# Performance work log

Hardware: AMD Instinct MI355X
Metric: run time of the kernel (lower is better)

The kernel has to match this reference:

```python
import jax, jax.numpy as jnp
import numpy as np

B, S, D = 1, 2048, 2048
N_HEADS, N_KV_HEADS = 32, 8
HEAD_DIM = D // N_HEADS  # 64
N_REP = N_HEADS // N_KV_HEADS  # 4


def setup_inputs() -> dict:
    key = jax.random.key(0)
    ks = jax.random.split(key, 6)
    x = jax.random.normal(ks[0], (B, S, D), dtype=jnp.float32)
    # weights stored as [in, out] so projection is x @ W
    wq = jax.random.normal(ks[1], (D, N_HEADS * HEAD_DIM), dtype=jnp.float32) * 0.02
    wk = jax.random.normal(ks[2], (D, N_KV_HEADS * HEAD_DIM), dtype=jnp.float32) * 0.02
    wv = jax.random.normal(ks[3], (D, N_KV_HEADS * HEAD_DIM), dtype=jnp.float32) * 0.02
    wo = jax.random.normal(ks[4], (N_HEADS * HEAD_DIM, D), dtype=jnp.float32) * 0.02
    # RoPE tables: freqs_cis has shape (seqlen, head_dim//2)
    theta = 10000.0
    inv_freq = 1.0 / (theta ** (jnp.arange(0, HEAD_DIM, 2, dtype=jnp.float32) / HEAD_DIM))
    angles = jnp.arange(S, dtype=jnp.float32)[:, None] * inv_freq[None, :]  # [S, hd/2]
    freqs_cos = jnp.cos(angles)
    freqs_sin = jnp.sin(angles)
    # causal additive mask, broadcast to [b, h, q, k]
    mask = jnp.triu(jnp.full((S, S), -jnp.inf, dtype=jnp.float32), k=1)[None, None]
    return {"x": x, "wq": wq, "wk": wk, "wv": wv, "wo": wo,
            "freqs_cos": freqs_cos, "freqs_sin": freqs_sin, "mask": mask}


def _apply_rope(t, cos, sin):
    # t: [B, S, H, head_dim]; pairs (t[...,2i], t[...,2i+1]) form complex numbers
    tr = t[..., 0::2]
    ti = t[..., 1::2]
    c = cos[None, :, None, :]
    s = sin[None, :, None, :]
    out_r = tr * c - ti * s
    out_i = tr * s + ti * c
    return jnp.stack([out_r, out_i], axis=-1).reshape(t.shape)


def reference(x, wq, wk, wv, wo, freqs_cos, freqs_sin, mask):
    bsz, seqlen, _ = x.shape
    xq = (x @ wq).reshape(bsz, seqlen, N_HEADS, HEAD_DIM)
    xk = (x @ wk).reshape(bsz, seqlen, N_KV_HEADS, HEAD_DIM)
    xv = (x @ wv).reshape(bsz, seqlen, N_KV_HEADS, HEAD_DIM)
    xq = _apply_rope(xq, freqs_cos, freqs_sin)
    xk = _apply_rope(xk, freqs_cos, freqs_sin)
    # repeat_kv (GQA expansion): [b,s,kvh,d] -> [b,s,h,d]
    keys = jnp.repeat(xk, N_REP, axis=2)
    values = jnp.repeat(xv, N_REP, axis=2)
    scale = 1.0 / np.sqrt(HEAD_DIM)
    # scores: [b, h, q, k]
    scores = jnp.einsum('bqhd,bkhd->bhqk', xq, keys) * scale
    scores = scores + mask
    probs = jax.nn.softmax(scores.astype(jnp.float32), axis=-1).astype(x.dtype)
    out = jnp.einsum('bhqk,bkhd->bqhd', probs, values)
    out = out.reshape(bsz, seqlen, N_HEADS * HEAD_DIM)
    return out @ wo
```

## Files before the change

### kernel.cpp

```cpp
#include <hip/hip_runtime.h>
#include <hip/hip_bf16.h>

#define S_LEN 2048
#define D_MODEL 2048
#define N_HEADS 32
#define N_KV 8
#define HEAD_DIM 64
#define KV_DIM (N_KV * HEAD_DIM)
#define QKV_N (D_MODEL + 2 * KV_DIM)

typedef __bf16 bf16_t;
typedef __attribute__((ext_vector_type(8))) __bf16 bf16x8;
typedef __attribute__((ext_vector_type(4))) float f32x4;
typedef __attribute__((ext_vector_type(16))) float f32x16;
typedef __attribute__((ext_vector_type(4))) unsigned int uint4v;
typedef __attribute__((ext_vector_type(2))) unsigned int uint2v;

__device__ __forceinline__ void gload_lds16(const void* g, void* l) {
    __builtin_amdgcn_global_load_lds(
        (const __attribute__((address_space(1))) unsigned char*)g,
        (__attribute__((address_space(3))) unsigned char*)l,
        16, 0, 0);
}

__global__ __launch_bounds__(256) void transpose_convert(const float* __restrict__ src,
                                                         __hip_bfloat16* __restrict__ dst,
                                                         int R, int C) {
    __shared__ float tile[32][33];
    const int bx = blockIdx.x * 32;
    const int by = blockIdx.y * 32;
    const int tx = threadIdx.x;
    const int ty = threadIdx.y;
#pragma unroll
    for (int i = 0; i < 32; i += 8)
        tile[ty + i][tx] = src[(size_t)(by + ty + i) * C + bx + tx];
    __syncthreads();
#pragma unroll
    for (int i = 0; i < 32; i += 8)
        dst[(size_t)(bx + ty + i) * R + by + tx] = __float2bfloat16(tile[tx][ty + i]);
}

__global__ __launch_bounds__(256) void convert_bf16(const float* __restrict__ src,
                                                    __hip_bfloat16* __restrict__ dst) {
    const int i = (blockIdx.x * 256 + threadIdx.x) * 8;
    const float4 a = *reinterpret_cast<const float4*>(src + i);
    const float4 b = *reinterpret_cast<const float4*>(src + i + 4);
    bf16x8 r;
    r[0] = (__bf16)a.x; r[1] = (__bf16)a.y; r[2] = (__bf16)a.z; r[3] = (__bf16)a.w;
    r[4] = (__bf16)b.x; r[5] = (__bf16)b.y; r[6] = (__bf16)b.z; r[7] = (__bf16)b.w;
    *reinterpret_cast<bf16x8*>(dst + i) = r;
}

__global__ __launch_bounds__(256) void rope_qk(__hip_bfloat16* __restrict__ t,
                                               const float* __restrict__ cos_t,
                                               const float* __restrict__ sin_t) {
    const int idx = blockIdx.x * blockDim.x + threadIdx.x;
    const int i = idx & 31;
    const int hh = (idx >> 5) % (N_HEADS + N_KV);
    const int s = idx / (32 * (N_HEADS + N_KV));
    const float c = cos_t[s * 32 + i];
    const float sn = sin_t[s * 32 + i];
    int col; float scale;
    if (hh < N_HEADS) { col = hh * HEAD_DIM + 2 * i; scale = 0.125f * 1.44269504f; }
    else { col = D_MODEL + (hh - N_HEADS) * HEAD_DIM + 2 * i; scale = 1.0f; }
    __hip_bfloat16* p = &t[(size_t)s * QKV_N + col];
    const float re = __bfloat162float(p[0]);
    const float im = __bfloat162float(p[1]);
    p[0] = __float2bfloat16((re * c - im * sn) * scale);
    p[1] = __float2bfloat16((re * sn + im * c) * scale);
}

__global__ __launch_bounds__(256) void transpose_v(const __hip_bfloat16* __restrict__ QKV,
                                                   __hip_bfloat16* __restrict__ Vt) {
    __shared__ __align__(16) __bf16 tile[64][72];
    const int s0 = blockIdx.x * 64;
    const int hkv = blockIdx.y;
    const int tid = threadIdx.x;
    {
        const int r = tid >> 2;
        const int c0 = (tid & 3) * 16;
        const __hip_bfloat16* src = QKV + (size_t)(s0 + r) * QKV_N + D_MODEL + KV_DIM + hkv * HEAD_DIM + c0;
        *reinterpret_cast<bf16x8*>(&tile[r][c0]) = *reinterpret_cast<const bf16x8*>(src);
        *reinterpret_cast<bf16x8*>(&tile[r][c0 + 8]) = *reinterpret_cast<const bf16x8*>(src + 8);
    }
    __syncthreads();
    {
        const int d = tid >> 2;
        const int sc = (tid & 3) * 16;
        bf16x8 o0, o1;
#pragma unroll
        for (int j = 0; j < 8; ++j) { o0[j] = tile[sc + j][d]; o1[j] = tile[sc + 8 + j][d]; }
        __hip_bfloat16* dst = Vt + (size_t)(hkv * HEAD_DIM + d) * S_LEN + s0 + sc;
        *reinterpret_cast<bf16x8*>(dst) = o0;
        *reinterpret_cast<bf16x8*>(dst + 8) = o1;
    }
}

__device__ inline void storeC(__hip_bfloat16* p, float v) { *p = __float2bfloat16(v); }
__device__ inline void storeC(float* p, float v) { *p = v; }

template <typename OutT>
__global__ __launch_bounds__(256) void gemm_bt(const __hip_bfloat16* __restrict__ A,
                                               const __hip_bfloat16* __restrict__ Bt,
                                               OutT* __restrict__ C,
                                               int M, int N, int K) {
    __shared__ __align__(16) __bf16 As[2][128 * 64];
    __shared__ __align__(16) __bf16 Bs[2][128 * 64];
    const int tid = threadIdx.x;
    const int w = tid >> 6, l = tid & 63;
    const int wr = w >> 1, wc = w & 1;
    const int l4 = l >> 4, l15 = l & 15;
    const int bm = blockIdx.y * 128, bn = blockIdx.x * 128;

    f32x4 acc[4][4];
#pragma unroll
    for (int i = 0; i < 4; ++i)
#pragma unroll
        for (int j = 0; j < 4; ++j) acc[i][j] = (f32x4){0.f, 0.f, 0.f, 0.f};

    auto stage = [&](int buf, int k0) {
#pragma unroll
        for (int p = 0; p < 4; ++p) {
            const int chunk = p * 256 + tid;
            const int row = chunk >> 3;
            const int cs = (chunk & 7) ^ (row & 7);
            gload_lds16(&A[(size_t)(bm + row) * K + k0 + cs * 8], &As[buf][chunk * 8]);
            gload_lds16(&Bt[(size_t)(bn + row) * K + k0 + cs * 8], &Bs[buf][chunk * 8]);
        }
    };

    const int nk = K >> 6;
    stage(0, 0);
    asm volatile("s_waitcnt vmcnt(0)" ::: "memory");
    __builtin_amdgcn_s_barrier();

#pragma unroll 2
    for (int kt = 0; kt < nk; ++kt) {
        const int cur = kt & 1;
        if (kt + 1 < nk) stage(cur ^ 1, (kt + 1) * 64);
#pragma unroll
        for (int ks = 0; ks < 2; ++ks) {
            bf16x8 a[4], b[4];
#pragma unroll
            for (int mi = 0; mi < 4; ++mi) {
                const int rr = wr * 64 + mi * 16 + l15;
                a[mi] = *reinterpret_cast<const bf16x8*>(
                    &As[cur][rr * 64 + (((ks * 4 + l4) ^ (rr & 7))) * 8]);
            }
#pragma unroll
            for (int ni = 0; ni < 4; ++ni) {
                const int rr = wc * 64 + ni * 16 + l15;
                b[ni] = *reinterpret_cast<const bf16x8*>(
                    &Bs[cur][rr * 64 + (((ks * 4 + l4) ^ (rr & 7))) * 8]);
            }
#pragma unroll
            for (int mi = 0; mi < 4; ++mi)
#pragma unroll
                for (int ni = 0; ni < 4; ++ni)
                    acc[mi][ni] = __builtin_amdgcn_mfma_f32_16x16x32_bf16(a[mi], b[ni], acc[mi][ni], 0, 0, 0);
        }
        asm volatile("s_waitcnt vmcnt(0)" ::: "memory");
        __builtin_amdgcn_s_barrier();
    }
#pragma unroll
    for (int mi = 0; mi < 4; ++mi)
#pragma unroll
        for (int ni = 0; ni < 4; ++ni)
#pragma unroll
            for (int r = 0; r < 4; ++r) {
                const int row = bm + wr * 64 + mi * 16 + l4 * 4 + r;
                const int col = bn + wc * 64 + ni * 16 + l15;
                storeC(&C[(size_t)row * N + col], acc[mi][ni][r]);
            }
}

#if __has_builtin(__builtin_amdgcn_permlane32_swap)
__device__ __forceinline__ void plswap(unsigned& x, unsigned& y, int) {
    uint2v r = __builtin_amdgcn_permlane32_swap(x, y, false, false);
    x = r[0]; y = r[1];
}
#else
__device__ __forceinline__ void plswap(unsigned& x, unsigned& y, int hi) {
    const unsigned px = __shfl_xor(x, 32, 64);
    const unsigned py = __shfl_xor(y, 32, 64);
    const unsigned nx = hi ? py : x;
    const unsigned ny = hi ? y : px;
    x = nx; y = ny;
}
#endif

__device__ __forceinline__ unsigned cvtpk_bf16(float lo, float hi) {
    unsigned w;
    asm("v_cvt_pk_bf16_f32 %0, %1, %2" : "=v"(w) : "v"(lo), "v"(hi));
    return w;
}
__device__ __forceinline__ float swap_max(float v, int hi) {
    unsigned x = __builtin_bit_cast(unsigned, v), y = x;
    plswap(x, y, hi);
    return fmaxf(__builtin_bit_cast(float, x), __builtin_bit_cast(float, y));
}
__device__ __forceinline__ float swap_add(float v, int hi) {
    unsigned x = __builtin_bit_cast(unsigned, v), y = x;
    plswap(x, y, hi);
    return __builtin_bit_cast(float, x) + __builtin_bit_cast(float, y);
}
template <int R0>
__device__ __forceinline__ bf16x8 build_pfrag(const f32x16& s, int hi) {
    unsigned A0 = cvtpk_bf16(s[R0 + 0], s[R0 + 1]);
    unsigned A1 = cvtpk_bf16(s[R0 + 2], s[R0 + 3]);
    unsigned B0 = cvtpk_bf16(s[R0 + 4], s[R0 + 5]);
    unsigned B1 = cvtpk_bf16(s[R0 + 6], s[R0 + 7]);
    plswap(A0, B0, hi);
    plswap(A1, B1, hi);
    uint4v u; u[0] = A0; u[1] = A1; u[2] = B0; u[3] = B1;
    return __builtin_bit_cast(bf16x8, u);
}

__global__ __launch_bounds__(512) void attn_kernel(const __hip_bfloat16* __restrict__ QKV,
                                                   const __hip_bfloat16* __restrict__ Vt,
                                                   __hip_bfloat16* __restrict__ O,
                                                   __hip_bfloat16* __restrict__ Opart,
                                                   float* __restrict__ ms,
                                                   int split) {
    const int h = blockIdx.y;
    const int hkv = h >> 2;
    int qc = 0, sl = 0, gbase = 0, ns = 1;
    if (!split) {
        qc = 7 - (int)blockIdx.x;
    } else {
        const int x = (int)blockIdx.x;
        int cum = 0;
#pragma unroll
        for (int q = 0; q < 8; ++q) {
            const int n = q + 1;
            if (x >= cum && x < cum + n) { qc = q; sl = x - cum; gbase = cum; }
            cum += n;
        }
        ns = qc + 1;
    }
    const int ntf = 4 * (qc + 1);
    const int t0 = split ? sl * 4 : 0;
    const int t1 = split ? min(t0 + 4, ntf) : ntf;

    const int tid = threadIdx.x;
    const int w = tid >> 6, l = tid & 63;
    const int lq = l & 31, hi = l >> 5;
    const int q0w = qc * 256 + w * 32;
    const int qlane = q0w + lq;

    __shared__ __align__(16) __bf16 Ks[2][64 * 64];
    __shared__ __align__(16) __bf16 Vs[2][64 * 64];

    const __hip_bfloat16* Kg = QKV + D_MODEL + hkv * HEAD_DIM;
    const __hip_bfloat16* Vg = Vt + (size_t)hkv * HEAD_DIM * S_LEN;

    auto stage = [&](int buf, int kv0) {
        const int chunk = tid;
        const int r = chunk >> 3;
        const int cs = (chunk & 7) ^ (r & 7);
        gload_lds16(&Kg[(size_t)(kv0 + r) * QKV_N + cs * 8], &Ks[buf][chunk * 8]);
        gload_lds16(&Vg[(size_t)r * S_LEN + kv0 + cs * 8], &Vs[buf][chunk * 8]);
    };

    bf16x8 qf[4];
#pragma unroll
    for (int f = 0; f < 4; ++f)
        qf[f] = *reinterpret_cast<const bf16x8*>(
            &QKV[(size_t)qlane * QKV_N + h * HEAD_DIM + 16 * f + 8 * hi]);

    f32x16 o0, o1;
#pragma unroll
    for (int r = 0; r < 16; ++r) { o0[r] = 0.f; o1[r] = 0.f; }
    float m_run = -__builtin_inff(), s_run = 0.f;

    stage(0, t0 * 64);

#pragma unroll 1
    for (int t = t0; t < t1; ++t) {
        __syncthreads();
        if (t + 1 < t1) stage((t + 1 - t0) & 1, (t + 1) * 64);
        const int kv0 = t * 64;
        if (kv0 <= q0w + 31) {
            const __bf16* Kb = Ks[(t - t0) & 1];
            const __bf16* Vb = Vs[(t - t0) & 1];

            f32x16 s0, s1;
#pragma unroll
            for (int r = 0; r < 16; ++r) { s0[r] = 0.f; s1[r] = 0.f; }
            __builtin_amdgcn_s_setprio(1);
#pragma unroll
            for (int f = 0; f < 4; ++f) {
                const int rr0 = lq;
                const int rr1 = 32 + lq;
                const bf16x8 ka0 = *reinterpret_cast<const bf16x8*>(
                    &Kb[rr0 * 64 + (((2 * f + hi) ^ (rr0 & 7))) * 8]);
                const bf16x8 ka1 = *reinterpret_cast<const bf16x8*>(
                    &Kb[rr1 * 64 + (((2 * f + hi) ^ (rr1 & 7))) * 8]);
                s0 = __builtin_amdgcn_mfma_f32_32x32x16_bf16(ka0, qf[f], s0, 0, 0, 0);
                s1 = __builtin_amdgcn_mfma_f32_32x32x16_bf16(ka1, qf[f], s1, 0, 0, 0);
            }
            __builtin_amdgcn_s_setprio(0);
            if (kv0 + 63 > q0w) {
#pragma unroll
                for (int r = 0; r < 16; ++r) {
                    const int kvb = (r & 3) + 8 * (r >> 2) + 4 * hi;
                    if (kv0 + kvb > qlane) s0[r] = -__builtin_inff();
                    if (kv0 + 32 + kvb > qlane) s1[r] = -__builtin_inff();
                }
            }
            float ta = fmaxf(s0[0], s1[0]), tb = fmaxf(s0[1], s1[1]);
            float tc = fmaxf(s0[2], s1[2]), td = fmaxf(s0[3], s1[3]);
#pragma unroll
            for (int r = 4; r < 16; r += 4) {
                ta = fmaxf(ta, fmaxf(s0[r], s1[r]));
                tb = fmaxf(tb, fmaxf(s0[r + 1], s1[r + 1]));
                tc = fmaxf(tc, fmaxf(s0[r + 2], s1[r + 2]));
                td = fmaxf(td, fmaxf(s0[r + 3], s1[r + 3]));
            }
            const float m_row = swap_max(fmaxf(fmaxf(ta, tb), fmaxf(tc, td)), hi);

            if (!__all(m_row <= m_run + 8.0f)) {
                const float mnew = fmaxf(m_run, m_row);
                const float corr = exp2f(m_run - mnew);
                m_run = mnew;
                s_run *= corr;
#pragma unroll
                for (int r = 0; r < 16; ++r) { o0[r] *= corr; o1[r] *= corr; }
            }
#pragma unroll
            for (int r = 0; r < 16; ++r) {
                s0[r] = exp2f(s0[r] - m_run);
                s1[r] = exp2f(s1[r] - m_run);
            }
            float ua = s0[0] + s1[0], ub = s0[1] + s1[1];
            float uc = s0[2] + s1[2], ud = s0[3] + s1[3];
#pragma unroll
            for (int r = 4; r < 16; r += 4) {
                ua += s0[r] + s1[r];
                ub += s0[r + 1] + s1[r + 1];
                uc += s0[r + 2] + s1[r + 2];
                ud += s0[r + 3] + s1[r + 3];
            }
            s_run += swap_add((ua + ub) + (uc + ud), hi);

            bf16x8 pa[4];
            pa[0] = build_pfrag<0>(s0, hi);
            pa[1] = build_pfrag<8>(s0, hi);
            pa[2] = build_pfrag<0>(s1, hi);
            pa[3] = build_pfrag<8>(s1, hi);

            __builtin_amdgcn_s_setprio(1);
#pragma unroll
            for (int ks = 0; ks < 4; ++ks) {
                const int rv0 = lq;
                const int rv1 = 32 + lq;
                const bf16x8 va0 = *reinterpret_cast<const bf16x8*>(
                    &Vb[rv0 * 64 + (((2 * ks + hi) ^ (rv0 & 7))) * 8]);
                const bf16x8 va1 = *reinterpret_cast<const bf16x8*>(
                    &Vb[rv1 * 64 + (((2 * ks + hi) ^ (rv1 & 7))) * 8]);
                o0 = __builtin_amdgcn_mfma_f32_32x32x16_bf16(va0, pa[ks], o0, 0, 0, 0);
                o1 = __builtin_amdgcn_mfma_f32_32x32x16_bf16(va1, pa[ks], o1, 0, 0, 0);
            }
            __builtin_amdgcn_s_setprio(0);
        }
    }

    if (ns == 1) {
        const float inv = 1.0f / s_run;
        __hip_bfloat16* orow = O + (size_t)qlane * D_MODEL + h * HEAD_DIM;
#pragma unroll
        for (int rr = 0; rr < 4; ++rr) {
            {
                uint2v u;
                u[0] = cvtpk_bf16(o0[4 * rr] * inv, o0[4 * rr + 1] * inv);
                u[1] = cvtpk_bf16(o0[4 * rr + 2] * inv, o0[4 * rr + 3] * inv);
                *reinterpret_cast<uint2v*>(orow + 8 * rr + 4 * hi) = u;
            }
            {
                uint2v u;
                u[0] = cvtpk_bf16(o1[4 * rr] * inv, o1[4 * rr + 1] * inv);
                u[1] = cvtpk_bf16(o1[4 * rr + 2] * inv, o1[4 * rr + 3] * inv);
                *reinterpret_cast<uint2v*>(orow + 32 + 8 * rr + 4 * hi) = u;
            }
        }
    } else {
        const int g = h * 36 + gbase + sl;
        const int row = w * 32 + lq;
        __hip_bfloat16* pb = Opart + ((size_t)g * 256 + row) * 64;
#pragma unroll
        for (int rr = 0; rr < 4; ++rr) {
            {
                uint2v u;
                u[0] = cvtpk_bf16(o0[4 * rr], o0[4 * rr + 1]);
                u[1] = cvtpk_bf16(o0[4 * rr + 2], o0[4 * rr + 3]);
                *reinterpret_cast<uint2v*>(pb + 8 * rr + 4 * hi) = u;
            }
            {
                uint2v u;
                u[0] = cvtpk_bf16(o1[4 * rr], o1[4 * rr + 1]);
                u[1] = cvtpk_bf16(o1[4 * rr + 2], o1[4 * rr + 3]);
                *reinterpret_cast<uint2v*>(pb + 32 + 8 * rr + 4 * hi) = u;
            }
        }
        if (hi == 0) {
            const size_t mi = (size_t)g * 256 + row;
            ms[mi * 2] = m_run;
            ms[mi * 2 + 1] = s_run;
        }
    }
}

__device__ __constant__ int kCum2[8] = {0, 1, 3, 6, 10, 15, 21, 28};

__global__ __launch_bounds__(256) void attn_merge(const __hip_bfloat16* __restrict__ Opart,
                                                  const float* __restrict__ ms,
                                                  __hip_bfloat16* __restrict__ O) {
    const int qc = 1 + blockIdx.x;
    const int h = blockIdx.z;
    const int tid = threadIdx.x;
    const int row = blockIdx.y * 32 + (tid >> 3);
    const int dv0 = (tid & 7) * 8;
    const int ns = qc + 1;
    const int g0 = h * 36 + kCum2[qc];

    float mv[8], sv[8];
    float M = -__builtin_inff();
#pragma unroll
    for (int s = 0; s < 8; ++s) {
        if (s < ns) {
            const size_t mi = (size_t)(g0 + s) * 256 + row;
            mv[s] = ms[mi * 2];
            sv[s] = ms[mi * 2 + 1];
            M = fmaxf(M, mv[s]);
        }
    }
    float S = 0.f;
    float acc[8];
#pragma unroll
    for (int j = 0; j < 8; ++j) acc[j] = 0.f;
#pragma unroll
    for (int s = 0; s < 8; ++s) {
        if (s < ns) {
            const float wgt = exp2f(mv[s] - M);
            S += wgt * sv[s];
            const bf16x8 v = *reinterpret_cast<const bf16x8*>(
                &Opart[((size_t)(g0 + s) * 256 + row) * 64 + dv0]);
#pragma unroll
            for (int j = 0; j < 8; ++j) acc[j] += wgt * (float)v[j];
        }
    }
    const float inv = 1.0f / S;
    uint4v u;
    u[0] = cvtpk_bf16(acc[0] * inv, acc[1] * inv);
    u[1] = cvtpk_bf16(acc[2] * inv, acc[3] * inv);
    u[2] = cvtpk_bf16(acc[4] * inv, acc[5] * inv);
    u[3] = cvtpk_bf16(acc[6] * inv, acc[7] * inv);
    *reinterpret_cast<uint4v*>(&O[(size_t)(qc * 256 + row) * D_MODEL + h * HEAD_DIM + dv0]) = u;
}

extern "C" void kernel_launch(void* const* d_in, const int* in_sizes, int n_in,
                              void* d_out, int out_size, void* d_ws, size_t ws_size,
                              hipStream_t stream) {
    const float* x  = (const float*)d_in[0];
    const float* wq = (const float*)d_in[1];
    const float* wk = (const float*)d_in[2];
    const float* wv = (const float*)d_in[3];
    const float* wo = (const float*)d_in[4];
    const float* fc = (const float*)d_in[5];
    const float* fs = (const float*)d_in[6];
    float* out = (float*)d_out;

    char* ws = (char*)d_ws;
    __hip_bfloat16* wqkvT = (__hip_bfloat16*)(ws);
    __hip_bfloat16* woT   = (__hip_bfloat16*)(ws + (12u << 20));
    __hip_bfloat16* attnb = (__hip_bfloat16*)(ws + (20u << 20));
    __hip_bfloat16* xb    = (__hip_bfloat16*)(ws + (28u << 20));
    __hip_bfloat16* QKV   = (__hip_bfloat16*)(ws + (36u << 20));
    __hip_bfloat16* Vt    = (__hip_bfloat16*)(ws + (48u << 20));
    float*          msb   = (float*)(ws + (50u << 20));
    __hip_bfloat16* Opart = (__hip_bfloat16*)(ws + (53u << 20));

    const int split = (ws_size >= (96ull << 20)) ? 1 : 0;

    const dim3 tb(32, 8);
    transpose_convert<<<dim3(D_MODEL / 32, D_MODEL / 32), tb, 0, stream>>>(wq, wqkvT, D_MODEL, D_MODEL);
    transpose_convert<<<dim3(KV_DIM / 32, D_MODEL / 32), tb, 0, stream>>>(wk, wqkvT + (size_t)D_MODEL * D_MODEL, D_MODEL, KV_DIM);
    transpose_convert<<<dim3(KV_DIM / 32, D_MODEL / 32), tb, 0, stream>>>(wv, wqkvT + (size_t)(D_MODEL + KV_DIM) * D_MODEL, D_MODEL, KV_DIM);
    transpose_convert<<<dim3(D_MODEL / 32, D_MODEL / 32), tb, 0, stream>>>(wo, woT, D_MODEL, D_MODEL);
    convert_bf16<<<(S_LEN * D_MODEL) / (256 * 8), 256, 0, stream>>>(x, xb);

    gemm_bt<__hip_bfloat16><<<dim3(QKV_N / 128, S_LEN / 128), 256, 0, stream>>>(xb, wqkvT, QKV, S_LEN, QKV_N, D_MODEL);

    rope_qk<<<(S_LEN * (N_HEADS + N_KV) * 32) / 256, 256, 0, stream>>>(QKV, fc, fs);

    transpose_v<<<dim3(S_LEN / 64, N_KV), 256, 0, stream>>>(QKV, Vt);

    if (split) {
        attn_kernel<<<dim3(36, N_HEADS), 512, 0, stream>>>(QKV, Vt, attnb, Opart, msb, 1);
        attn_merge<<<dim3(7, 8, N_HEADS), 256, 0, stream>>>(Opart, msb, attnb);
    } else {
        attn_kernel<<<dim3(8, N_HEADS), 512, 0, stream>>>(QKV, Vt, attnb, Opart, msb, 0);
    }

    gemm_bt<float><<<dim3(D_MODEL / 128, S_LEN / 128), 256, 0, stream>>>(attnb, woT, out, S_LEN, D_MODEL, D_MODEL);

    (void)in_sizes; (void)n_in; (void)out_size;
}
```

Baseline: 156.2 us.

## Use triple-buffered K=32 tiles with partial vmcnt waits in bf16 GEMM

```diff
diff --git a/kernel.cpp b/kernel.cpp
--- a/kernel.cpp
+++ b/kernel.cpp
@@ -99,13 +99,13 @@
 __device__ inline void storeC(__hip_bfloat16* p, float v) { *p = __float2bfloat16(v); }
 __device__ inline void storeC(float* p, float v) { *p = v; }
 
-template <typename OutT>
+template <typename OutT, int KK>
 __global__ __launch_bounds__(256) void gemm_bt(const __hip_bfloat16* __restrict__ A,
                                                const __hip_bfloat16* __restrict__ Bt,
                                                OutT* __restrict__ C,
-                                               int M, int N, int K) {
-    __shared__ __align__(16) __bf16 As[2][128 * 64];
-    __shared__ __align__(16) __bf16 Bs[2][128 * 64];
+                                               int M, int N) {
+    __shared__ __align__(16) __bf16 As[3][128 * 32];
+    __shared__ __align__(16) __bf16 Bs[3][128 * 32];
     const int tid = threadIdx.x;
     const int w = tid >> 6, l = tid & 63;
     const int wr = w >> 1, wc = w & 1;
@@ -118,49 +118,50 @@
 #pragma unroll
         for (int j = 0; j < 4; ++j) acc[i][j] = (f32x4){0.f, 0.f, 0.f, 0.f};
 
+    const int r0 = tid >> 2;
+    const int cc0 = tid & 3;
+
     auto stage = [&](int buf, int k0) {
 #pragma unroll
-        for (int p = 0; p < 4; ++p) {
-            const int chunk = p * 256 + tid;
-            const int row = chunk >> 3;
-            const int cs = (chunk & 7) ^ (row & 7);
-            gload_lds16(&A[(size_t)(bm + row) * K + k0 + cs * 8], &As[buf][chunk * 8]);
-            gload_lds16(&Bt[(size_t)(bn + row) * K + k0 + cs * 8], &Bs[buf][chunk * 8]);
+        for (int p = 0; p < 2; ++p) {
+            const int row = p * 64 + r0;
+            const int cs = cc0 ^ (row & 3);
+            gload_lds16(&A[(size_t)(bm + row) * KK + k0 + cs * 8], &As[buf][(p * 256 + tid) * 8]);
+            gload_lds16(&Bt[(size_t)(bn + row) * KK + k0 + cs * 8], &Bs[buf][(p * 256 + tid) * 8]);
         }
     };
 
-    const int nk = K >> 6;
+    constexpr int nk = KK >> 5;
     stage(0, 0);
-    asm volatile("s_waitcnt vmcnt(0)" ::: "memory");
+    stage(1, 32);
+    asm volatile("s_waitcnt vmcnt(4)" ::: "memory");
     __builtin_amdgcn_s_barrier();
 
-#pragma unroll 2
+#pragma unroll
     for (int kt = 0; kt < nk; ++kt) {
-        const int cur = kt & 1;
-        if (kt + 1 < nk) stage(cur ^ 1, (kt + 1) * 64);
-#pragma unroll
-        for (int ks = 0; ks < 2; ++ks) {
-            bf16x8 a[4], b[4];
-#pragma unroll
-            for (int mi = 0; mi < 4; ++mi) {
-                const int rr = wr * 64 + mi * 16 + l15;
-                a[mi] = *reinterpret_cast<const bf16x8*>(
-                    &As[cur][rr * 64 + (((ks * 4 + l4) ^ (rr & 7))) * 8]);
-            }
-#pragma unroll
-            for (int ni = 0; ni < 4; ++ni) {
-                const int rr = wc * 64 + ni * 16 + l15;
-                b[ni] = *reinterpret_cast<const bf16x8*>(
-                    &Bs[cur][rr * 64 + (((ks * 4 + l4) ^ (rr & 7))) * 8]);
-            }
-#pragma unroll
-            for (int mi = 0; mi < 4; ++mi)
-#pragma unroll
-                for (int ni = 0; ni < 4; ++ni)
-                    acc[mi][ni] = __builtin_amdgcn_mfma_f32_16x16x32_bf16(a[mi], b[ni], acc[mi][ni], 0, 0, 0);
-        }
-        asm volatile("s_waitcnt vmcnt(0)" ::: "memory");
-        __builtin_amdgcn_s_barrier();
+        if (kt + 2 < nk) stage((kt + 2) % 3, (kt + 2) * 32);
+        const int cur = kt % 3;
+        bf16x8 a[4], b[4];
+#pragma unroll
+        for (int mi = 0; mi < 4; ++mi) {
+            const int rr = wr * 64 + mi * 16 + l15;
+            a[mi] = *reinterpret_cast<const bf16x8*>(&As[cur][rr * 32 + ((l4 ^ (rr & 3))) * 8]);
+        }
+#pragma unroll
+        for (int ni = 0; ni < 4; ++ni) {
+            const int rr = wc * 64 + ni * 16 + l15;
+            b[ni] = *reinterpret_cast<const bf16x8*>(&Bs[cur][rr * 32 + ((l4 ^ (rr & 3))) * 8]);
+        }
+#pragma unroll
+        for (int mi = 0; mi < 4; ++mi)
+#pragma unroll
+            for (int ni = 0; ni < 4; ++ni)
+                acc[mi][ni] = __builtin_amdgcn_mfma_f32_16x16x32_bf16(a[mi], b[ni], acc[mi][ni], 0, 0, 0);
+        if (kt + 1 < nk) {
+            if (kt + 2 < nk) asm volatile("s_waitcnt vmcnt(4)" ::: "memory");
+            else             asm volatile("s_waitcnt vmcnt(0)" ::: "memory");
+            __builtin_amdgcn_s_barrier();
+        }
     }
 #pragma unroll
     for (int mi = 0; mi < 4; ++mi)
@@ -489,7 +490,7 @@
     transpose_convert<<<dim3(D_MODEL / 32, D_MODEL / 32), tb, 0, stream>>>(wo, woT, D_MODEL, D_MODEL);
     convert_bf16<<<(S_LEN * D_MODEL) / (256 * 8), 256, 0, stream>>>(x, xb);
 
-    gemm_bt<__hip_bfloat16><<<dim3(QKV_N / 128, S_LEN / 128), 256, 0, stream>>>(xb, wqkvT, QKV, S_LEN, QKV_N, D_MODEL);
+    gemm_bt<__hip_bfloat16, 2048><<<dim3(QKV_N / 128, S_LEN / 128), 256, 0, stream>>>(xb, wqkvT, QKV, S_LEN, QKV_N);
 
     rope_qk<<<(S_LEN * (N_HEADS + N_KV) * 32) / 256, 256, 0, stream>>>(QKV, fc, fs);
 
@@ -502,7 +503,7 @@
         attn_kernel<<<dim3(8, N_HEADS), 512, 0, stream>>>(QKV, Vt, attnb, Opart, msb, 0);
     }
 
-    gemm_bt<float><<<dim3(D_MODEL / 128, S_LEN / 128), 256, 0, stream>>>(attnb, woT, out, S_LEN, D_MODEL, D_MODEL);
+    gemm_bt<float, 2048><<<dim3(D_MODEL / 128, S_LEN / 128), 256, 0, stream>>>(attnb, woT, out, S_LEN, D_MODEL);
 
     (void)in_sizes; (void)n_in; (void)out_size;
 }
```

Result: slower. 159.7 us (+2.3%).
